# Kernel optimization log

Hardware: AMD Instinct MI355X
Metric: run time of the kernel (lower is better)

Reference implementation:

```python
import jax, jax.numpy as jnp
import numpy as np

K, C, H, W, B = 128, 128, 24, 8, 32
HW = H * W
EPS = 1e-5


def setup_inputs() -> dict:
    key = jax.random.key(0)
    ks = jax.random.split(key, 4)
    feature = jax.random.normal(ks[0], (B, C, H, W), dtype=jnp.float32)
    target = jax.random.randint(ks[1], (B,), 0, K, dtype=jnp.int64)
    class_memory = jax.random.normal(ks[2], (K, C, H, W), dtype=jnp.float32)
    bn_gamma = jnp.ones((1,), jnp.float32)
    bn_beta = jnp.zeros((1,), jnp.float32)
    fc_w = jax.random.normal(ks[3], (1, 2 * HW), dtype=jnp.float32) / np.sqrt(2 * HW)
    fc_b = jnp.zeros((1,), jnp.float32)
    logit_gamma = jnp.ones((1,), jnp.float32)
    logit_beta = jnp.zeros((1,), jnp.float32)
    return {"feature": feature, "target": target, "class_memory": class_memory,
            "bn_gamma": bn_gamma, "bn_beta": bn_beta, "fc_w": fc_w, "fc_b": fc_b,
            "logit_gamma": logit_gamma, "logit_beta": logit_beta}


def _bn_all(x, gamma, beta):
    # BatchNorm1d with 1 channel in training mode: stats over ALL elements
    mean = x.mean()
    var = ((x - mean) ** 2).mean()  # biased variance, as torch uses for normalization
    return (x - mean) * jax.lax.rsqrt(var + EPS) * gamma[0] + beta[0]


def reference(feature, target, class_memory, bn_gamma, bn_beta, fc_w, fc_b,
              logit_gamma, logit_beta):
    f = feature.reshape(B, C, HW)        # query: [B, C, hw]
    m = class_memory.reshape(K, C, HW)   # memory: [K, C, hw]
    # correlation volume: score[k,b,q,p] = sum_c f[b,c,q] * m[k,c,p]
    corr = jnp.einsum('bcq,kcp->kbqp', f, m)  # [K, B, hw, hw]
    # dual-axis max pooling: best-match over query locs and over memory locs
    score = jnp.concatenate([corr.max(axis=2), corr.max(axis=3)], axis=-1)  # [K,B,2hw]
    score = _bn_all(score, bn_gamma, bn_beta)
    # FC to single logit per (class, sample)
    logits = score.reshape(K * B, 2 * HW) @ fc_w.T + fc_b  # [K*B, 1]
    logits = logits.reshape(K, B).T                         # [B, K]
    logits = _bn_all(logits, logit_gamma, logit_beta)
    # focal binary cross-entropy with logits
    onehot = jax.nn.one_hot(target, K, dtype=logits.dtype)  # [B, K]
    bce = onehot * jax.nn.softplus(-logits) + (1.0 - onehot) * jax.nn.softplus(logits)
    prob = jax.nn.sigmoid(logits)
    weight = jnp.where(onehot > 0.5, 1.0 - prob, prob) ** 2
    loss = (bce * weight).sum(-1)  # [B]
    preds = jnp.argmax(logits, axis=1)
    acc = (preds == target).astype(jnp.float32)
    return loss, acc
```

## Files before the change

### kernel.cpp

```cpp
#include <hip/hip_runtime.h>
#include <math.h>

#define BB 32
#define CCH 128
#define KK 128
#define HWW 192
#define NKB (KK * BB)
#define P2 (2 * HWW)

typedef __attribute__((ext_vector_type(8))) __bf16 bf16x8;
typedef __attribute__((ext_vector_type(16))) float f32x16;

#define A_ELEMS (BB * 8 * 6 * 512)
#define B_ELEMS (KK * 16 * 6 * 512)

__global__ __launch_bounds__(256) void pack_kernel(
    const float* __restrict__ feature,
    const float* __restrict__ class_memory,
    __bf16* __restrict__ A2,
    __bf16* __restrict__ B2)
{
    int gid = blockIdx.x * 256 + threadIdx.x;
    if (gid < 98304) {
        int l = gid & 63;
        int r = gid >> 6;
        int t = r % 6;  r /= 6;
        int ks = r & 7;
        int e = r >> 3;
        const float* src = feature + (size_t)e * CCH * HWW;
        int c0 = ks * 16 + (l >> 5) * 8;
        int q  = t * 32 + (l & 31);
        bf16x8 v;
#pragma unroll
        for (int j = 0; j < 8; ++j) v[j] = (__bf16)src[(c0 + j) * HWW + q];
        *(bf16x8*)(A2 + ((size_t)(e * 8 + ks) * 6 + t) * 512 + l * 8) = v;
    } else {
        int g2 = gid - 98304;
        int l = g2 & 63;
        int r = g2 >> 6;
        int t = r % 6;  r /= 6;
        int ks = r & 7;
        int e = r >> 3;
        const float* src = class_memory + (size_t)e * CCH * HWW;
        int c0 = ks * 16 + (l >> 5) * 8;
        int q  = t * 32 + (l & 31);
        bf16x8 vh, vl;
#pragma unroll
        for (int j = 0; j < 8; ++j) {
            float x = src[(c0 + j) * HWW + q];
            __bf16 h = (__bf16)x;
            vh[j] = h;
            vl[j] = (__bf16)(x - (float)h);
        }
        __bf16* base = B2 + ((size_t)e * 16 + ks) * 3072 + t * 512 + l * 8;
        *(bf16x8*)base = vh;
        *(bf16x8*)(base + 8 * 3072) = vl;
    }
}

__global__ __launch_bounds__(384, 3) void corr_mfma(
    const __bf16* __restrict__ A2,
    const __bf16* __restrict__ B2,
    const float* __restrict__ fc_w,
    float* __restrict__ dot_sw,
    float* __restrict__ psum,
    float* __restrict__ psq)
{
    __shared__ __align__(16) char smem[40320];
    __bf16 (*lds)[12][64][8] = (__bf16 (*)[12][64][8])smem;

    const int tid = threadIdx.x;
    const int l   = tid & 63;
    const int w   = tid >> 6;
    const int wy  = w / 3;
    const int wx  = w % 3;
    const int hi  = l >> 5;

    const int bid = blockIdx.x;
    const int kb  = (bid & 7) * 512 + (bid >> 3);
    const int k   = kb >> 5;
    const int b   = kb & 31;

    f32x16 acc[3][2];
#pragma unroll
    for (int i = 0; i < 3; ++i)
#pragma unroll
        for (int j = 0; j < 2; ++j)
#pragma unroll
            for (int rr = 0; rr < 16; ++rr) acc[i][j][rr] = 0.f;

    const __bf16* aw = A2 + (size_t)b * 24576 + wy * 1536 + l * 8;
    const __bf16* bsrc = B2 + (size_t)k * 49152 +
                         (w < 3 ? w * 1024 : 24576 + (w - 3) * 1024);

    auto loadA = [&](bf16x8* dst, int g) {
        const __bf16* ap = aw + (size_t)g * 3072;
        dst[0] = *(const bf16x8*)(ap);
        dst[1] = *(const bf16x8*)(ap + 512);
        dst[2] = *(const bf16x8*)(ap + 1024);
    };
    auto stageB = [&](int buf2, int g) {
        const char* src = (const char*)(bsrc + (size_t)g * 3072) + l * 16;
        __builtin_amdgcn_global_load_lds(
            (const __attribute__((address_space(1))) void*)src,
            (__attribute__((address_space(3))) void*)&lds[buf2][2 * w][0][0],
            16, 0, 0);
        __builtin_amdgcn_global_load_lds(
            (const __attribute__((address_space(1))) void*)(src + 1024),
            (__attribute__((address_space(3))) void*)&lds[buf2][2 * w + 1][0][0],
            16, 0, 0);
    };
    auto compute = [&](int buf2, bf16x8* a) {
        bf16x8 bh0 = *(const bf16x8*)&lds[buf2][wx * 2][l][0];
        bf16x8 bh1 = *(const bf16x8*)&lds[buf2][wx * 2 + 1][l][0];
        bf16x8 bl0 = *(const bf16x8*)&lds[buf2][6 + wx * 2][l][0];
        bf16x8 bl1 = *(const bf16x8*)&lds[buf2][6 + wx * 2 + 1][l][0];
#pragma unroll
        for (int i = 0; i < 3; ++i) {
            acc[i][0] = __builtin_amdgcn_mfma_f32_32x32x16_bf16(a[i], bh0, acc[i][0], 0, 0, 0);
            acc[i][0] = __builtin_amdgcn_mfma_f32_32x32x16_bf16(a[i], bl0, acc[i][0], 0, 0, 0);
            acc[i][1] = __builtin_amdgcn_mfma_f32_32x32x16_bf16(a[i], bh1, acc[i][1], 0, 0, 0);
            acc[i][1] = __builtin_amdgcn_mfma_f32_32x32x16_bf16(a[i], bl1, acc[i][1], 0, 0, 0);
        }
    };

    bf16x8 aA[3], aB[3];
    loadA(aA, 0);
    stageB(0, 0);
    __syncthreads();
#pragma unroll
    for (int g = 0; g < 8; ++g) {
        bf16x8* acur = (g & 1) ? aB : aA;
        bf16x8* anxt = (g & 1) ? aA : aB;
        if (g < 7) {
            stageB((g & 1) ^ 1, g + 1);
            loadA(anxt, g + 1);
        }
        compute(g & 1, acur);
        __syncthreads();
    }

    float cm[2];
#pragma unroll
    for (int j = 0; j < 2; ++j) {
        float m = -INFINITY;
#pragma unroll
        for (int i = 0; i < 3; ++i)
#pragma unroll
            for (int rr = 0; rr < 16; ++rr) m = fmaxf(m, acc[i][j][rr]);
        cm[j] = m;
    }
#pragma unroll
    for (int j = 0; j < 2; ++j) cm[j] = fmaxf(cm[j], __shfl_xor(cm[j], 32));

    float rm[3][16];
#pragma unroll
    for (int i = 0; i < 3; ++i)
#pragma unroll
        for (int rr = 0; rr < 16; ++rr)
            rm[i][rr] = fmaxf(acc[i][0][rr], acc[i][1][rr]);

    float* rowpart = (float*)smem;
    float* scores  = (float*)smem + 9312;
    float* colred  = (float*)smem + 9696;

    if (l < 32) {
#pragma unroll
        for (int j = 0; j < 2; ++j)
            colred[wy * 192 + wx * 64 + j * 32 + l] = cm[j];
    }
    if (wy == 0) {
#pragma unroll
        for (int i = 0; i < 3; ++i)
#pragma unroll
            for (int rr = 0; rr < 16; ++rr) {
                int q = i * 32 + (rr & 3) + 8 * (rr >> 2) + 4 * hi;
                rowpart[q * 97 + wx * 32 + (l & 31)] = rm[i][rr];
            }
    }
    __syncthreads();
    if (tid < 192) scores[tid] = fmaxf(colred[tid], colred[192 + tid]);
    {
        int q = tid >> 2, part = tid & 3;
        float v = -INFINITY;
#pragma unroll
        for (int c = 0; c < 24; ++c) v = fmaxf(v, rowpart[q * 97 + part * 24 + c]);
        v = fmaxf(v, __shfl_xor(v, 1));
        v = fmaxf(v, __shfl_xor(v, 2));
        if (part == 0) scores[192 + q] = v;
    }
    __syncthreads();
    if (wy == 1) {
#pragma unroll
        for (int i = 0; i < 3; ++i)
#pragma unroll
            for (int rr = 0; rr < 16; ++rr) {
                int q = i * 32 + (rr & 3) + 8 * (rr >> 2) + 4 * hi;
                rowpart[q * 97 + wx * 32 + (l & 31)] = rm[i][rr];
            }
    }
    __syncthreads();
    {
        int q = tid >> 2, part = tid & 3;
        float v = -INFINITY;
#pragma unroll
        for (int c = 0; c < 24; ++c) v = fmaxf(v, rowpart[q * 97 + part * 24 + c]);
        v = fmaxf(v, __shfl_xor(v, 1));
        v = fmaxf(v, __shfl_xor(v, 2));
        if (part == 0) scores[192 + 96 + q] = v;
    }
    __syncthreads();

    if (tid < 64) {
        float ds = 0.f, s1 = 0.f, s2 = 0.f;
#pragma unroll
        for (int u = 0; u < 6; ++u) {
            int j = tid + 64 * u;
            float s = scores[j];
            float ww = fc_w[j];
            ds = fmaf(s, ww, ds);
            s1 += s;
            s2 = fmaf(s, s, s2);
        }
        for (int off = 32; off > 0; off >>= 1) {
            ds += __shfl_down(ds, off);
            s1 += __shfl_down(s1, off);
            s2 += __shfl_down(s2, off);
        }
        if (tid == 0) { dot_sw[kb] = ds; psum[kb] = s1; psq[kb] = s2; }
    }
}

__device__ __forceinline__ float softplusf(float x) {
    return fmaxf(x, 0.f) + log1pf(expf(-fabsf(x)));
}

__device__ __forceinline__ float block_sum1024(float v, float* tmp) {
    __syncthreads();
    for (int off = 32; off > 0; off >>= 1) v += __shfl_down(v, off);
    if ((threadIdx.x & 63) == 0) tmp[threadIdx.x >> 6] = v;
    __syncthreads();
    float r = 0.f;
#pragma unroll
    for (int i = 0; i < 16; ++i) r += tmp[i];
    return r;
}

__global__ __launch_bounds__(1024) void finalize_kernel(
    const float* __restrict__ dot_sw,
    const float* __restrict__ psum,
    const float* __restrict__ psq,
    const float* __restrict__ fc_w,
    const float* __restrict__ fc_b,
    const float* __restrict__ bn_gamma,
    const float* __restrict__ bn_beta,
    const float* __restrict__ logit_gamma,
    const float* __restrict__ logit_beta,
    const int* __restrict__ target,
    float* __restrict__ out)
{
    const int tid = threadIdx.x;
    __shared__ float l_s[NKB];
    __shared__ float tmp[16];

    float s1 = 0.f, s2 = 0.f, sw = 0.f;
#pragma unroll
    for (int u = 0; u < 4; ++u) {
        int i = tid + 1024 * u;
        s1 += psum[i];
        s2 += psq[i];
    }
    if (tid < P2) sw = fc_w[tid];

    float S1 = block_sum1024(s1, tmp);
    float S2 = block_sum1024(s2, tmp);
    float SW = block_sum1024(sw, tmp);

    const float N1 = (float)NKB * (float)P2;
    float mean1 = S1 / N1;
    float var1  = S2 / N1 - mean1 * mean1;
    float cA = bn_gamma[0] * rsqrtf(var1 + 1e-5f);
    float cB = (bn_beta[0] - cA * mean1) * SW + fc_b[0];

    float lr[4];
    float t1 = 0.f, t2 = 0.f;
#pragma unroll
    for (int u = 0; u < 4; ++u) {
        int i = tid + 1024 * u;
        lr[u] = fmaf(cA, dot_sw[i], cB);
        t1 += lr[u];
        t2 = fmaf(lr[u], lr[u], t2);
    }
    float T1 = block_sum1024(t1, tmp);
    float T2 = block_sum1024(t2, tmp);
    float mean2 = T1 / (float)NKB;
    float var2  = T2 / (float)NKB - mean2 * mean2;
    float cC = logit_gamma[0] * rsqrtf(var2 + 1e-5f);
    float cD = logit_beta[0] - mean2 * cC;

#pragma unroll
    for (int u = 0; u < 4; ++u) {
        int i = tid + 1024 * u;
        l_s[i] = fmaf(lr[u], cC, cD);
    }
    __syncthreads();

    const int b  = tid >> 5;
    const int tt = tid & 31;
    const int tgt = target[b];
    float loss  = 0.f;
    float bestv = -INFINITY;
    int   bestk = 0x7fffffff;
#pragma unroll
    for (int u = 0; u < 4; ++u) {
        int kk = tt + 32 * u;
        float lg = l_s[kk * BB + b];
        float prob = 1.f / (1.f + expf(-lg));
        bool pos = (kk == tgt);
        float wgt = pos ? (1.f - prob) : prob;
        float bce = pos ? softplusf(-lg) : softplusf(lg);
        loss += bce * wgt * wgt;
        if (lg > bestv) { bestv = lg; bestk = kk; }
        else if (lg == bestv && kk < bestk) bestk = kk;
    }
    for (int off = 16; off > 0; off >>= 1) {
        loss += __shfl_down(loss, off, 32);
        float ov = __shfl_down(bestv, off, 32);
        int   ok = __shfl_down(bestk, off, 32);
        if (ov > bestv) { bestv = ov; bestk = ok; }
        else if (ov == bestv && ok < bestk) bestk = ok;
    }
    if (tt == 0) {
        out[b]      = loss;
        out[BB + b] = (bestk == tgt) ? 1.f : 0.f;
    }
}

extern "C" void kernel_launch(void* const* d_in, const int* in_sizes, int n_in,
                              void* d_out, int out_size, void* d_ws, size_t ws_size,
                              hipStream_t stream)
{
    const float* feature      = (const float*)d_in[0];
    const int*   target       = (const int*)d_in[1];
    const float* class_memory = (const float*)d_in[2];
    const float* bn_gamma     = (const float*)d_in[3];
    const float* bn_beta      = (const float*)d_in[4];
    const float* fc_w         = (const float*)d_in[5];
    const float* fc_b         = (const float*)d_in[6];
    const float* logit_gamma  = (const float*)d_in[7];
    const float* logit_beta   = (const float*)d_in[8];
    float* out = (float*)d_out;

    __bf16* A2 = (__bf16*)d_ws;
    __bf16* B2 = A2 + A_ELEMS;
    float* dot_sw = (float*)(B2 + B_ELEMS);
    float* psum   = dot_sw + NKB;
    float* psq    = psum + NKB;

    pack_kernel<<<1920, 256, 0, stream>>>(feature, class_memory, A2, B2);
    corr_mfma<<<NKB, 384, 0, stream>>>(A2, B2, fc_w, dot_sw, psum, psq);
    finalize_kernel<<<1, 1024, 0, stream>>>(dot_sw, psum, psq, fc_w, fc_b,
                                            bn_gamma, bn_beta,
                                            logit_gamma, logit_beta,
                                            target, out);
}
```

Before: 204.5 us.

## Make correlation blocks loop over batch samples with high-half memory held in registers

```diff
diff --git a/kernel.cpp b/kernel.cpp
--- a/kernel.cpp
+++ b/kernel.cpp
@@ -58,7 +58,9 @@
     }
 }
 
-__global__ __launch_bounds__(384, 3) void corr_mfma(
+#define MFMA32(A, B, C) __builtin_amdgcn_mfma_f32_32x32x16_bf16((A), (B), (C), 0, 0, 0)
+
+__global__ __launch_bounds__(768, 3) void corr_mfma(
     const __bf16* __restrict__ A2,
     const __bf16* __restrict__ B2,
     const float* __restrict__ fc_w,
@@ -66,168 +68,141 @@
     float* __restrict__ psum,
     float* __restrict__ psq)
 {
-    __shared__ __align__(16) char smem[40320];
-    __bf16 (*lds)[12][64][8] = (__bf16 (*)[12][64][8])smem;
+    __shared__ __align__(16) __bf16 A_lds[8][6][64][8];
+    __shared__ __align__(16) __bf16 Blo_lds[8][6][64][8];
+    __shared__ float colpart[2][192];
+    __shared__ float rowpart[6][192];
+    __shared__ float scores[384];
 
     const int tid = threadIdx.x;
     const int l   = tid & 63;
+    const int lc  = l & 31;
     const int w   = tid >> 6;
-    const int wy  = w / 3;
-    const int wx  = w % 3;
-    const int hi  = l >> 5;
-
-    const int bid = blockIdx.x;
-    const int kb  = (bid & 7) * 512 + (bid >> 3);
-    const int k   = kb >> 5;
-    const int b   = kb & 31;
-
-    f32x16 acc[3][2];
-#pragma unroll
-    for (int i = 0; i < 3; ++i)
-#pragma unroll
-        for (int j = 0; j < 2; ++j)
-#pragma unroll
-            for (int rr = 0; rr < 16; ++rr) acc[i][j][rr] = 0.f;
-
-    const __bf16* aw = A2 + (size_t)b * 24576 + wy * 1536 + l * 8;
-    const __bf16* bsrc = B2 + (size_t)k * 49152 +
-                         (w < 3 ? w * 1024 : 24576 + (w - 3) * 1024);
-
-    auto loadA = [&](bf16x8* dst, int g) {
-        const __bf16* ap = aw + (size_t)g * 3072;
-        dst[0] = *(const bf16x8*)(ap);
-        dst[1] = *(const bf16x8*)(ap + 512);
-        dst[2] = *(const bf16x8*)(ap + 1024);
+    const int wy  = w / 6;
+    const int wx  = w % 6;
+
+    const int bid   = blockIdx.x;
+    const int xcd   = bid & 7;
+    const int slot  = bid >> 3;
+    const int k     = xcd * 16 + (slot >> 1);
+    const int bhalf = slot & 1;
+
+    const __bf16* bkbase = B2 + (size_t)k * 49152;
+    bf16x8 bh[8];
+#pragma unroll
+    for (int g = 0; g < 8; ++g)
+        bh[g] = *(const bf16x8*)(bkbase + g * 3072 + wx * 512 + l * 8);
+
+    float fcw[6];
+#pragma unroll
+    for (int u = 0; u < 6; ++u) fcw[u] = fc_w[l + 64 * u];
+
+    const char* lobase = (const char*)B2 + (size_t)k * 98304 + 49152;
+    const char* abase  = (const char*)A2;
+    char* lodst = (char*)&Blo_lds[0][0][0][0];
+    char* adst  = (char*)&A_lds[0][0][0][0];
+    const int woff = w * 1024 + l * 16;
+    const int wbase = w * 1024;
+
+    auto stageA = [&](int b) {
+        const char* src = abase + (size_t)b * 49152;
+#pragma unroll
+        for (int i = 0; i < 4; ++i)
+            __builtin_amdgcn_global_load_lds(
+                (const __attribute__((address_space(1))) void*)(src + i * 12288 + woff),
+                (__attribute__((address_space(3))) void*)(adst + i * 12288 + wbase),
+                16, 0, 0);
     };
-    auto stageB = [&](int buf2, int g) {
-        const char* src = (const char*)(bsrc + (size_t)g * 3072) + l * 16;
+#pragma unroll
+    for (int i = 0; i < 4; ++i)
         __builtin_amdgcn_global_load_lds(
-            (const __attribute__((address_space(1))) void*)src,
-            (__attribute__((address_space(3))) void*)&lds[buf2][2 * w][0][0],
+            (const __attribute__((address_space(1))) void*)(lobase + i * 12288 + woff),
+            (__attribute__((address_space(3))) void*)(lodst + i * 12288 + wbase),
             16, 0, 0);
-        __builtin_amdgcn_global_load_lds(
-            (const __attribute__((address_space(1))) void*)(src + 1024),
-            (__attribute__((address_space(3))) void*)&lds[buf2][2 * w + 1][0][0],
-            16, 0, 0);
-    };
-    auto compute = [&](int buf2, bf16x8* a) {
-        bf16x8 bh0 = *(const bf16x8*)&lds[buf2][wx * 2][l][0];
-        bf16x8 bh1 = *(const bf16x8*)&lds[buf2][wx * 2 + 1][l][0];
-        bf16x8 bl0 = *(const bf16x8*)&lds[buf2][6 + wx * 2][l][0];
-        bf16x8 bl1 = *(const bf16x8*)&lds[buf2][6 + wx * 2 + 1][l][0];
+    stageA(bhalf * 16);
+    __syncthreads();
+
+    for (int bi = 0; bi < 16; ++bi) {
+        const int b = bhalf * 16 + bi;
+
+        f32x16 acc[3], acc2[3];
+#pragma unroll
+        for (int i = 0; i < 3; ++i)
+#pragma unroll
+            for (int rr = 0; rr < 16; ++rr) { acc[i][rr] = 0.f; acc2[i][rr] = 0.f; }
+
+#pragma unroll
+        for (int g = 0; g < 8; ++g) {
+            bf16x8 a0 = *(const bf16x8*)&A_lds[g][wy * 3 + 0][l][0];
+            bf16x8 a1 = *(const bf16x8*)&A_lds[g][wy * 3 + 1][l][0];
+            bf16x8 a2 = *(const bf16x8*)&A_lds[g][wy * 3 + 2][l][0];
+            bf16x8 bl = *(const bf16x8*)&Blo_lds[g][wx][l][0];
+            acc[0]  = MFMA32(a0, bh[g], acc[0]);
+            acc[0]  = MFMA32(a0, bl,    acc[0]);
+            acc[1]  = MFMA32(a1, bh[g], acc[1]);
+            acc[1]  = MFMA32(a1, bl,    acc[1]);
+            acc[2]  = MFMA32(a2, bh[g], acc[2]);
+            acc[2]  = MFMA32(a2, bl,    acc[2]);
+            acc2[0] = MFMA32(bh[g], a0, acc2[0]);
+            acc2[0] = MFMA32(bl,    a0, acc2[0]);
+            acc2[1] = MFMA32(bh[g], a1, acc2[1]);
+            acc2[1] = MFMA32(bl,    a1, acc2[1]);
+            acc2[2] = MFMA32(bh[g], a2, acc2[2]);
+            acc2[2] = MFMA32(bl,    a2, acc2[2]);
+        }
+
+        float cmv = -INFINITY;
+#pragma unroll
+        for (int i = 0; i < 3; ++i)
+#pragma unroll
+            for (int rr = 0; rr < 16; ++rr) cmv = fmaxf(cmv, acc[i][rr]);
+        cmv = fmaxf(cmv, __shfl_xor(cmv, 32));
+        if (l < 32) colpart[wy][wx * 32 + lc] = cmv;
+
 #pragma unroll
         for (int i = 0; i < 3; ++i) {
-            acc[i][0] = __builtin_amdgcn_mfma_f32_32x32x16_bf16(a[i], bh0, acc[i][0], 0, 0, 0);
-            acc[i][0] = __builtin_amdgcn_mfma_f32_32x32x16_bf16(a[i], bl0, acc[i][0], 0, 0, 0);
-            acc[i][1] = __builtin_amdgcn_mfma_f32_32x32x16_bf16(a[i], bh1, acc[i][1], 0, 0, 0);
-            acc[i][1] = __builtin_amdgcn_mfma_f32_32x32x16_bf16(a[i], bl1, acc[i][1], 0, 0, 0);
-        }
-    };
-
-    bf16x8 aA[3], aB[3];
-    loadA(aA, 0);
-    stageB(0, 0);
-    __syncthreads();
-#pragma unroll
-    for (int g = 0; g < 8; ++g) {
-        bf16x8* acur = (g & 1) ? aB : aA;
-        bf16x8* anxt = (g & 1) ? aA : aB;
-        if (g < 7) {
-            stageB((g & 1) ^ 1, g + 1);
-            loadA(anxt, g + 1);
-        }
-        compute(g & 1, acur);
+            float t = -INFINITY;
+#pragma unroll
+            for (int rr = 0; rr < 16; ++rr) t = fmaxf(t, acc2[i][rr]);
+            t = fmaxf(t, __shfl_xor(t, 32));
+            if (l < 32) rowpart[wx][(wy * 3 + i) * 32 + lc] = t;
+        }
         __syncthreads();
-    }
-
-    float cm[2];
-#pragma unroll
-    for (int j = 0; j < 2; ++j) {
-        float m = -INFINITY;
-#pragma unroll
-        for (int i = 0; i < 3; ++i)
-#pragma unroll
-            for (int rr = 0; rr < 16; ++rr) m = fmaxf(m, acc[i][j][rr]);
-        cm[j] = m;
-    }
-#pragma unroll
-    for (int j = 0; j < 2; ++j) cm[j] = fmaxf(cm[j], __shfl_xor(cm[j], 32));
-
-    float rm[3][16];
-#pragma unroll
-    for (int i = 0; i < 3; ++i)
-#pragma unroll
-        for (int rr = 0; rr < 16; ++rr)
-            rm[i][rr] = fmaxf(acc[i][0][rr], acc[i][1][rr]);
-
-    float* rowpart = (float*)smem;
-    float* scores  = (float*)smem + 9312;
-    float* colred  = (float*)smem + 9696;
-
-    if (l < 32) {
-#pragma unroll
-        for (int j = 0; j < 2; ++j)
-            colred[wy * 192 + wx * 64 + j * 32 + l] = cm[j];
-    }
-    if (wy == 0) {
-#pragma unroll
-        for (int i = 0; i < 3; ++i)
-#pragma unroll
-            for (int rr = 0; rr < 16; ++rr) {
-                int q = i * 32 + (rr & 3) + 8 * (rr >> 2) + 4 * hi;
-                rowpart[q * 97 + wx * 32 + (l & 31)] = rm[i][rr];
+
+        if (bi < 15) stageA(b + 1);
+
+        if (tid < 192) {
+            scores[tid] = fmaxf(colpart[0][tid], colpart[1][tid]);
+        } else if (tid < 384) {
+            int q = tid - 192;
+            float v = rowpart[0][q];
+#pragma unroll
+            for (int x = 1; x < 6; ++x) v = fmaxf(v, rowpart[x][q]);
+            scores[192 + q] = v;
+        }
+        __syncthreads();
+
+        if (tid < 64) {
+            float ds = 0.f, s1 = 0.f, s2 = 0.f;
+#pragma unroll
+            for (int u = 0; u < 6; ++u) {
+                float s = scores[l + 64 * u];
+                ds = fmaf(s, fcw[u], ds);
+                s1 += s;
+                s2 = fmaf(s, s, s2);
             }
-    }
-    __syncthreads();
-    if (tid < 192) scores[tid] = fmaxf(colred[tid], colred[192 + tid]);
-    {
-        int q = tid >> 2, part = tid & 3;
-        float v = -INFINITY;
-#pragma unroll
-        for (int c = 0; c < 24; ++c) v = fmaxf(v, rowpart[q * 97 + part * 24 + c]);
-        v = fmaxf(v, __shfl_xor(v, 1));
-        v = fmaxf(v, __shfl_xor(v, 2));
-        if (part == 0) scores[192 + q] = v;
-    }
-    __syncthreads();
-    if (wy == 1) {
-#pragma unroll
-        for (int i = 0; i < 3; ++i)
-#pragma unroll
-            for (int rr = 0; rr < 16; ++rr) {
-                int q = i * 32 + (rr & 3) + 8 * (rr >> 2) + 4 * hi;
-                rowpart[q * 97 + wx * 32 + (l & 31)] = rm[i][rr];
+            for (int off = 32; off > 0; off >>= 1) {
+                ds += __shfl_down(ds, off);
+                s1 += __shfl_down(s1, off);
+                s2 += __shfl_down(s2, off);
             }
-    }
-    __syncthreads();
-    {
-        int q = tid >> 2, part = tid & 3;
-        float v = -INFINITY;
-#pragma unroll
-        for (int c = 0; c < 24; ++c) v = fmaxf(v, rowpart[q * 97 + part * 24 + c]);
-        v = fmaxf(v, __shfl_xor(v, 1));
-        v = fmaxf(v, __shfl_xor(v, 2));
-        if (part == 0) scores[192 + 96 + q] = v;
-    }
-    __syncthreads();
-
-    if (tid < 64) {
-        float ds = 0.f, s1 = 0.f, s2 = 0.f;
-#pragma unroll
-        for (int u = 0; u < 6; ++u) {
-            int j = tid + 64 * u;
-            float s = scores[j];
-            float ww = fc_w[j];
-            ds = fmaf(s, ww, ds);
-            s1 += s;
-            s2 = fmaf(s, s, s2);
-        }
-        for (int off = 32; off > 0; off >>= 1) {
-            ds += __shfl_down(ds, off);
-            s1 += __shfl_down(s1, off);
-            s2 += __shfl_down(s2, off);
-        }
-        if (tid == 0) { dot_sw[kb] = ds; psum[kb] = s1; psq[kb] = s2; }
+            if (tid == 0) {
+                int kb = k * 32 + b;
+                dot_sw[kb] = ds;
+                psum[kb]   = s1;
+                psq[kb]    = s2;
+            }
+        }
     }
 }
 
@@ -358,7 +333,7 @@
     float* psq    = psum + NKB;
 
     pack_kernel<<<1920, 256, 0, stream>>>(feature, class_memory, A2, B2);
-    corr_mfma<<<NKB, 384, 0, stream>>>(A2, B2, fc_w, dot_sw, psum, psq);
+    corr_mfma<<<256, 768, 0, stream>>>(A2, B2, fc_w, dot_sw, psum, psq);
     finalize_kernel<<<1, 1024, 0, stream>>>(dot_sw, psum, psq, fc_w, fc_b,
                                             bn_gamma, bn_beta,
                                             logit_gamma, logit_beta,
```

Result: faster. 198.8 us (-2.8%).
